# Kernel tuning notes

Measured on AMD Instinct MI355X. Metric: run time of the kernel, lower is better.

The kernel has to match this reference:

```python
import jax, jax.numpy as jnp
import numpy as np

T, B, I, H, O = 512, 64, 256, 512, 256

def setup_inputs() -> dict:
    key = jax.random.key(0)
    ks = jax.random.split(key, 7)
    s_ih = 1.0 / np.sqrt(H)
    return {
        "x": jax.random.normal(ks[0], (T, B, I), dtype=jnp.float32),
        "W_ih": jax.random.uniform(ks[1], (H, I), jnp.float32, -s_ih, s_ih),
        "W_hh": jax.random.uniform(ks[2], (H, H), jnp.float32, -s_ih, s_ih),
        "b_ih": jax.random.uniform(ks[3], (H,), jnp.float32, -s_ih, s_ih),
        "b_hh": jax.random.uniform(ks[4], (H,), jnp.float32, -s_ih, s_ih),
        "W_out": jax.random.uniform(ks[5], (O, H), jnp.float32, -s_ih, s_ih),
        "b_out": jax.random.uniform(ks[6], (O,), jnp.float32, -s_ih, s_ih),
    }

def reference(x, W_ih, W_hh, b_ih, b_hh, W_out, b_out):
    # Precompute input projection for all timesteps: [T, B, H]
    xp = jnp.einsum('tbi,hi->tbh', x, W_ih) + b_ih + b_hh

    def step(h, xp_t):
        h_new = jnp.tanh(xp_t + h @ W_hh.T)
        return h_new, h_new

    h0 = jnp.zeros((x.shape[1], W_hh.shape[0]), dtype=x.dtype)
    h_last, rnn_out = jax.lax.scan(step, h0, xp)  # rnn_out: [T, B, H]
    y = jnp.einsum('tbh,oh->tbo', rnn_out, W_out) + b_out
    return y, h_last[None]  # h: [1, B, H] matching torch nn.RNN
```

## Files before the change

### kernel.cpp

```cpp
#include <hip/hip_runtime.h>

#define T_DIM 512
#define B_DIM 64
#define I_DIM 256
#define H_DIM 512
#define O_DIM 256

typedef __attribute__((ext_vector_type(8))) short short8;
typedef __attribute__((ext_vector_type(4))) float f32x4;

__device__ __forceinline__ unsigned short f2bf(float f){
  unsigned int u = __builtin_bit_cast(unsigned int, f);
  u += 0x7fffu + ((u >> 16) & 1u);
  return (unsigned short)(u >> 16);
}
__device__ __forceinline__ float bf2f(unsigned short b){
  unsigned int u = ((unsigned int)b) << 16;
  return __builtin_bit_cast(float, u);
}

#if defined(__has_builtin)
#if __has_builtin(__builtin_amdgcn_sdot4)
#define HAVE_SDOT4 1
#endif
#if __has_builtin(__builtin_amdgcn_update_dpp)
#define HAVE_DPP 1
#endif
#endif

__device__ __forceinline__ int sdot4(int a, int b, int c){
#ifdef HAVE_SDOT4
  return __builtin_amdgcn_sdot4(a, b, c, false);
#else
  #pragma unroll
  for (int i = 0; i < 4; ++i){
    c += (int)(signed char)(a >> (8*i) & 0xff) * (int)(signed char)(b >> (8*i) & 0xff);
  }
  return c;
#endif
}

__global__ void pack_bf16(const float* __restrict__ x,
                          const float* __restrict__ wih,
                          const float* __restrict__ wout,
                          unsigned short* __restrict__ xb,
                          unsigned short* __restrict__ wihb,
                          unsigned short* __restrict__ woutb){
  const int NX = (T_DIM*B_DIM*I_DIM)/4;
  const int NW = (H_DIM*I_DIM)/4;
  int i = blockIdx.x * 256 + threadIdx.x;
  const float4* src; unsigned short* dst; int j;
  if (i < NX)          { src = (const float4*)x;    dst = xb;    j = i; }
  else if (i < NX+NW)  { src = (const float4*)wih;  dst = wihb;  j = i - NX; }
  else                 { src = (const float4*)wout; dst = woutb; j = i - NX - NW; }
  float4 f = src[j];
  ushort4 v;
  v.x = f2bf(f.x); v.y = f2bf(f.y); v.z = f2bf(f.z); v.w = f2bf(f.w);
  ((ushort4*)dst)[j] = v;
}

__global__ void quant_whh(const float* __restrict__ W, int* __restrict__ Wq){
  int p = blockIdx.x * blockDim.x + threadIdx.x;
  const float s  = 0.04419417382415922f;
  const float qs = 127.0f / s;
  int out = 0;
  #pragma unroll
  for (int i = 0; i < 4; ++i){
    float w = W[(size_t)p*4 + i];
    int q = __float2int_rn(w * qs);
    q = q < -127 ? -127 : (q > 127 ? 127 : q);
    out |= (q & 0xff) << (8*i);
  }
  Wq[p] = out;
}

__global__
__attribute__((amdgpu_flat_work_group_size(512, 512), amdgpu_waves_per_eu(2, 2)))
void rnn_recur(
    const int* __restrict__ Wq,
    const unsigned short* __restrict__ xp,
    unsigned short* __restrict__ rnn,
    float* __restrict__ hlast)
{
  __shared__ union {
    int  hq[2][128];
    char occupancy_cap[84 * 1024];
  } sm;
  const int b   = blockIdx.x;
  const int tid = threadIdx.x;
  const int g   = tid >> 3;
  const int c   = tid & 7;
  const int cc  = c & 3;
  const int rr  = c >> 2;

  int w[4][32];
  #pragma unroll
  for (int i = 0; i < 4; ++i){
    const uint4* wp = (const uint4*)(Wq + (size_t)(8*g + 4*rr + i)*128 + 32*cc);
    #pragma unroll
    for (int k = 0; k < 8; ++k){
      uint4 v = wp[k];
      w[i][4*k+0] = (int)v.x; w[i][4*k+1] = (int)v.y;
      w[i][4*k+2] = (int)v.z; w[i][4*k+3] = (int)v.w;
    }
  }
  if (tid < 256) ((int*)sm.hq)[tid] = 0;

  const int D    = tid >> 2;
  const int wloc = D ^ (((D >> 5) & 3) << 2);

  int ko[8];
  #pragma unroll
  for (int k = 0; k < 8; ++k) ko[k] = 8*cc + (k ^ cc);

  const float kscale = 0.04419417382415922f / (127.0f * 127.0f);
  const int BH = B_DIM * H_DIM;

  float xp_next = bf2f(xp[(size_t)b*H_DIM + tid]);
  float h = 0.0f;
  __syncthreads();

  for (int t = 0; t < T_DIM; ++t){
    float xp_cur = xp_next;
    {
      int tn = (t + 1 < T_DIM) ? (t + 1) : t;
      xp_next = bf2f(xp[(size_t)tn*BH + (size_t)b*H_DIM + tid]);
    }
    const uint4* hb = (const uint4*)sm.hq[t & 1];
    uint4 hv[8];
    #pragma unroll
    for (int k = 0; k < 8; ++k) hv[k] = hb[ko[k]];

    int acc[4];
    #pragma unroll
    for (int i = 0; i < 4; ++i) acc[i] = 0;
    #pragma unroll
    for (int i = 0; i < 4; ++i){
      #pragma unroll
      for (int k = 0; k < 8; ++k){
        acc[i] = sdot4(w[i][4*k+0], (int)hv[k].x, acc[i]);
        acc[i] = sdot4(w[i][4*k+1], (int)hv[k].y, acc[i]);
        acc[i] = sdot4(w[i][4*k+2], (int)hv[k].z, acc[i]);
        acc[i] = sdot4(w[i][4*k+3], (int)hv[k].w, acc[i]);
      }
    }
#ifdef HAVE_DPP
    #pragma unroll
    for (int i = 0; i < 4; ++i){
      acc[i] += __builtin_amdgcn_update_dpp(0, acc[i], 0xB1, 0xf, 0xf, true);
      acc[i] += __builtin_amdgcn_update_dpp(0, acc[i], 0x4E, 0xf, 0xf, true);
    }
#else
    #pragma unroll
    for (int i = 0; i < 4; ++i){
      acc[i] += __shfl_xor(acc[i], 1);
      acc[i] += __shfl_xor(acc[i], 2);
    }
#endif
    int t0 = (c & 1) ? acc[1] : acc[0];
    int t1 = (c & 1) ? acc[3] : acc[2];
    int am = (c & 2) ? t1 : t0;

    float pre = xp_cur + (float)am * kscale;
    float aa = fabsf(pre);
    float e  = __expf(-2.0f * aa);
    float r  = (1.0f - e) * __builtin_amdgcn_rcpf(1.0f + e);
    h = copysignf(r, pre);

    rnn[(size_t)t*BH + (size_t)b*H_DIM + tid] = f2bf(h);

    int q = __float2int_rn(h * 127.0f) & 0xff;
#ifdef HAVE_DPP
    int p1 = __builtin_amdgcn_update_dpp(0, q, 0xB1, 0xf, 0xf, true);
    int y  = q | (p1 << 8);
    int p2 = __builtin_amdgcn_update_dpp(0, y, 0x4E, 0xf, 0xf, true);
    int z  = y | (p2 << 16);
    if ((tid & 3) == 0) sm.hq[(t + 1) & 1][wloc] = z;
#else
    ((char*)sm.hq[(t + 1) & 1])[wloc*4 + (tid & 3)] = (char)q;
#endif
    __syncthreads();
  }
  hlast[(size_t)b*H_DIM + tid] = h;
}

template<typename TA, typename TB, typename TO>
__global__ __launch_bounds__(256) void gemm_bt(
    const TA* __restrict__ A, const TB* __restrict__ B, TO* __restrict__ C,
    const float* __restrict__ bias1, const float* __restrict__ bias2,
    int M, int N, int K)
{
  __shared__ unsigned short As[64][40];
  __shared__ unsigned short Bs[64][40];
  const int tid  = threadIdx.x;
  const int m0   = blockIdx.y * 64;
  const int n0   = blockIdx.x * 64;
  const int srow = tid >> 2, skc = tid & 3;
  const int lane = tid & 63, wid = tid >> 6;
  const int wm   = wid >> 1, wn = wid & 1;
  const int lr   = lane & 15, lq = lane >> 4;

  f32x4 acc[2][2];
  #pragma unroll
  for (int i = 0; i < 2; ++i)
    #pragma unroll
    for (int j = 0; j < 2; ++j) acc[i][j] = (f32x4){0.f, 0.f, 0.f, 0.f};

  for (int k0 = 0; k0 < K; k0 += 32){
    {
      const TA* src = A + (size_t)(m0 + srow)*K + k0 + skc*8;
      uint4 v;
      if constexpr (__is_same(TA, float)){
        float4 f0 = *(const float4*)src;
        float4 f1 = *(const float4*)(src + 4);
        v.x = (unsigned)f2bf(f0.x) | ((unsigned)f2bf(f0.y) << 16);
        v.y = (unsigned)f2bf(f0.z) | ((unsigned)f2bf(f0.w) << 16);
        v.z = (unsigned)f2bf(f1.x) | ((unsigned)f2bf(f1.y) << 16);
        v.w = (unsigned)f2bf(f1.z) | ((unsigned)f2bf(f1.w) << 16);
      } else {
        v = *(const uint4*)src;
      }
      *(uint4*)&As[srow][skc*8] = v;
    }
    {
      const TB* src = B + (size_t)(n0 + srow)*K + k0 + skc*8;
      uint4 v;
      if constexpr (__is_same(TB, float)){
        float4 f0 = *(const float4*)src;
        float4 f1 = *(const float4*)(src + 4);
        v.x = (unsigned)f2bf(f0.x) | ((unsigned)f2bf(f0.y) << 16);
        v.y = (unsigned)f2bf(f0.z) | ((unsigned)f2bf(f0.w) << 16);
        v.z = (unsigned)f2bf(f1.x) | ((unsigned)f2bf(f1.y) << 16);
        v.w = (unsigned)f2bf(f1.z) | ((unsigned)f2bf(f1.w) << 16);
      } else {
        v = *(const uint4*)src;
      }
      *(uint4*)&Bs[srow][skc*8] = v;
    }
    __syncthreads();
    uint4 av0 = *(const uint4*)&As[wm*32      + lr][lq*8];
    uint4 av1 = *(const uint4*)&As[wm*32 + 16 + lr][lq*8];
    uint4 bv0 = *(const uint4*)&Bs[wn*32      + lr][lq*8];
    uint4 bv1 = *(const uint4*)&Bs[wn*32 + 16 + lr][lq*8];
    short8 a0 = __builtin_bit_cast(short8, av0);
    short8 a1 = __builtin_bit_cast(short8, av1);
    short8 b0 = __builtin_bit_cast(short8, bv0);
    short8 b1 = __builtin_bit_cast(short8, bv1);
    acc[0][0] = __builtin_amdgcn_mfma_f32_16x16x32_bf16(a0, b0, acc[0][0], 0, 0, 0);
    acc[0][1] = __builtin_amdgcn_mfma_f32_16x16x32_bf16(a0, b1, acc[0][1], 0, 0, 0);
    acc[1][0] = __builtin_amdgcn_mfma_f32_16x16x32_bf16(a1, b0, acc[1][0], 0, 0, 0);
    acc[1][1] = __builtin_amdgcn_mfma_f32_16x16x32_bf16(a1, b1, acc[1][1], 0, 0, 0);
    __syncthreads();
  }

  #pragma unroll
  for (int i = 0; i < 2; ++i)
    #pragma unroll
    for (int j = 0; j < 2; ++j)
      #pragma unroll
      for (int r = 0; r < 4; ++r){
        int grow = m0 + wm*32 + i*16 + lq*4 + r;
        int gcol = n0 + wn*32 + j*16 + lr;
        float v = acc[i][j][r] + bias1[gcol];
        if (bias2) v += bias2[gcol];
        if constexpr (__is_same(TO, float)) C[(size_t)grow*N + gcol] = v;
        else                                C[(size_t)grow*N + gcol] = f2bf(v);
      }
}

extern "C" void kernel_launch(void* const* d_in, const int* in_sizes, int n_in,
                              void* d_out, int out_size, void* d_ws, size_t ws_size,
                              hipStream_t stream){
  (void)in_sizes; (void)n_in; (void)out_size; (void)ws_size;
  const float* x    = (const float*)d_in[0];
  const float* Wih  = (const float*)d_in[1];
  const float* Whh  = (const float*)d_in[2];
  const float* bih  = (const float*)d_in[3];
  const float* bhh  = (const float*)d_in[4];
  const float* Wout = (const float*)d_in[5];
  const float* bout = (const float*)d_in[6];
  float* y     = (float*)d_out;
  float* hlast = y + (size_t)T_DIM * B_DIM * O_DIM;

  char* ws = (char*)d_ws;
  const size_t MB = 1024*1024;
  unsigned short* xp   = (unsigned short*)ws;
  unsigned short* rnn  = (unsigned short*)(ws + 32*MB);
  unsigned short* xb   = (unsigned short*)(ws + 32*MB);
  unsigned short* wihb = (unsigned short*)(ws + 48*MB);
  int*            Wq   = (int*)           (ws + 64*MB);
  unsigned short* wob  = (unsigned short*)(ws + 64*MB + 256*1024);

  pack_bf16<<<8448, 256, 0, stream>>>(x, Wih, Wout, xb, wihb, wob);
  quant_whh<<<256, 256, 0, stream>>>(Whh, Wq);
  gemm_bt<unsigned short, unsigned short, unsigned short><<<dim3(8, 512), 256, 0, stream>>>(
      xb, wihb, xp, bih, bhh, T_DIM*B_DIM, H_DIM, I_DIM);
  rnn_recur<<<64, 512, 0, stream>>>(Wq, xp, rnn, hlast);
  gemm_bt<unsigned short, unsigned short, float><<<dim3(4, 512), 256, 0, stream>>>(
      rnn, wob, y, bout, nullptr, T_DIM*B_DIM, O_DIM, H_DIM);
}
```

Baseline: 542.6 us.

## Use int8 MFMA for recurrent matvec instead of sdot4 with DPP reduction

Replaces the per-thread sdot4 dot products and DPP cross-lane reductions in the sequential RNN step with int8 16x16x64 MFMA instructions. The quantized W_hh rows are held in registers as MFMA A-fragments, and the hidden state is broadcast as the B operand. Results are picked out of the accumulator lanes and rearranged with a shuffle. Because only one column of each MFMA carries useful data (batch 1 per block), most of the matrix throughput goes unused. The gain depends on cutting per-step latency on the serial critical path.

Result: faster. 524.2 us (-3.4%).

```diff
diff --git a/kernel.cpp b/kernel.cpp
--- a/kernel.cpp
+++ b/kernel.cpp
@@ -8,6 +8,7 @@
 
 typedef __attribute__((ext_vector_type(8))) short short8;
 typedef __attribute__((ext_vector_type(4))) float f32x4;
+typedef __attribute__((ext_vector_type(4))) int   i32x4;
 
 __device__ __forceinline__ unsigned short f2bf(float f){
   unsigned int u = __builtin_bit_cast(unsigned int, f);
@@ -20,25 +21,10 @@
 }
 
 #if defined(__has_builtin)
-#if __has_builtin(__builtin_amdgcn_sdot4)
-#define HAVE_SDOT4 1
-#endif
 #if __has_builtin(__builtin_amdgcn_update_dpp)
 #define HAVE_DPP 1
 #endif
 #endif
-
-__device__ __forceinline__ int sdot4(int a, int b, int c){
-#ifdef HAVE_SDOT4
-  return __builtin_amdgcn_sdot4(a, b, c, false);
-#else
-  #pragma unroll
-  for (int i = 0; i < 4; ++i){
-    c += (int)(signed char)(a >> (8*i) & 0xff) * (int)(signed char)(b >> (8*i) & 0xff);
-  }
-  return c;
-#endif
-}
 
 __global__ void pack_bf16(const float* __restrict__ x,
                           const float* __restrict__ wih,
@@ -83,35 +69,29 @@
     float* __restrict__ hlast)
 {
   __shared__ union {
-    int  hq[2][128];
+    char H[2][512];
     char occupancy_cap[84 * 1024];
   } sm;
-  const int b   = blockIdx.x;
-  const int tid = threadIdx.x;
-  const int g   = tid >> 3;
-  const int c   = tid & 7;
-  const int cc  = c & 3;
-  const int rr  = c >> 2;
-
-  int w[4][32];
-  #pragma unroll
-  for (int i = 0; i < 4; ++i){
-    const uint4* wp = (const uint4*)(Wq + (size_t)(8*g + 4*rr + i)*128 + 32*cc);
-    #pragma unroll
-    for (int k = 0; k < 8; ++k){
-      uint4 v = wp[k];
-      w[i][4*k+0] = (int)v.x; w[i][4*k+1] = (int)v.y;
-      w[i][4*k+2] = (int)v.z; w[i][4*k+3] = (int)v.w;
-    }
-  }
-  if (tid < 256) ((int*)sm.hq)[tid] = 0;
-
-  const int D    = tid >> 2;
-  const int wloc = D ^ (((D >> 5) & 3) << 2);
-
-  int ko[8];
-  #pragma unroll
-  for (int k = 0; k < 8; ++k) ko[k] = 8*cc + (k ^ cc);
+  const int b    = blockIdx.x;
+  const int tid  = threadIdx.x;
+  const int lane = tid & 63;
+  const int wv   = tid >> 6;
+  const int lr   = lane & 15;
+  const int hi   = lane >> 4;
+
+  i32x4 wf[4][8];
+  const char* Wb = (const char*)Wq;
+  #pragma unroll
+  for (int rt = 0; rt < 4; ++rt){
+    const char* rowp = Wb + (size_t)(64*wv + 16*rt + lr)*512 + hi*16;
+    #pragma unroll
+    for (int kt = 0; kt < 8; ++kt)
+      wf[rt][kt] = *(const i32x4*)(rowp + (size_t)kt*64);
+  }
+
+  if (tid < 256) ((int*)sm.H)[tid] = 0;
+
+  const int src = (((lane >> 2) & 3) << 4) | ((lane >> 4) << 2) | (lane & 3);
 
   const float kscale = 0.04419417382415922f / (127.0f * 127.0f);
   const int BH = B_DIM * H_DIM;
@@ -126,40 +106,37 @@
       int tn = (t + 1 < T_DIM) ? (t + 1) : t;
       xp_next = bf2f(xp[(size_t)tn*BH + (size_t)b*H_DIM + tid]);
     }
-    const uint4* hb = (const uint4*)sm.hq[t & 1];
-    uint4 hv[8];
-    #pragma unroll
-    for (int k = 0; k < 8; ++k) hv[k] = hb[ko[k]];
-
-    int acc[4];
-    #pragma unroll
-    for (int i = 0; i < 4; ++i) acc[i] = 0;
-    #pragma unroll
-    for (int i = 0; i < 4; ++i){
-      #pragma unroll
-      for (int k = 0; k < 8; ++k){
-        acc[i] = sdot4(w[i][4*k+0], (int)hv[k].x, acc[i]);
-        acc[i] = sdot4(w[i][4*k+1], (int)hv[k].y, acc[i]);
-        acc[i] = sdot4(w[i][4*k+2], (int)hv[k].z, acc[i]);
-        acc[i] = sdot4(w[i][4*k+3], (int)hv[k].w, acc[i]);
-      }
-    }
-#ifdef HAVE_DPP
-    #pragma unroll
-    for (int i = 0; i < 4; ++i){
-      acc[i] += __builtin_amdgcn_update_dpp(0, acc[i], 0xB1, 0xf, 0xf, true);
-      acc[i] += __builtin_amdgcn_update_dpp(0, acc[i], 0x4E, 0xf, 0xf, true);
-    }
-#else
-    #pragma unroll
-    for (int i = 0; i < 4; ++i){
-      acc[i] += __shfl_xor(acc[i], 1);
-      acc[i] += __shfl_xor(acc[i], 2);
-    }
-#endif
-    int t0 = (c & 1) ? acc[1] : acc[0];
-    int t1 = (c & 1) ? acc[3] : acc[2];
-    int am = (c & 2) ? t1 : t0;
+
+    const char* Hc = sm.H[t & 1];
+    i32x4 a0 = {0,0,0,0}, a1 = {0,0,0,0}, a2 = {0,0,0,0}, a3 = {0,0,0,0};
+    #pragma unroll
+    for (int kt = 0; kt < 8; ++kt){
+      i32x4 bf = *(const i32x4*)(Hc + kt*64 + hi*16);
+      a0 = __builtin_amdgcn_mfma_i32_16x16x64_i8(wf[0][kt], bf, a0, 0, 0, 0);
+      a1 = __builtin_amdgcn_mfma_i32_16x16x64_i8(wf[1][kt], bf, a1, 0, 0, 0);
+      a2 = __builtin_amdgcn_mfma_i32_16x16x64_i8(wf[2][kt], bf, a2, 0, 0, 0);
+      a3 = __builtin_amdgcn_mfma_i32_16x16x64_i8(wf[3][kt], bf, a3, 0, 0, 0);
+    }
+
+    int f0, f1, f2, f3;
+    {
+      int e0 = (lane & 4) ? a1[0] : a0[0];
+      int e1 = (lane & 4) ? a3[0] : a2[0];
+      f0 = (lane & 8) ? e1 : e0;
+      e0 = (lane & 4) ? a1[1] : a0[1];
+      e1 = (lane & 4) ? a3[1] : a2[1];
+      f1 = (lane & 8) ? e1 : e0;
+      e0 = (lane & 4) ? a1[2] : a0[2];
+      e1 = (lane & 4) ? a3[2] : a2[2];
+      f2 = (lane & 8) ? e1 : e0;
+      e0 = (lane & 4) ? a1[3] : a0[3];
+      e1 = (lane & 4) ? a3[3] : a2[3];
+      f3 = (lane & 8) ? e1 : e0;
+    }
+    int g0 = (lane & 1) ? f1 : f0;
+    int g1 = (lane & 1) ? f3 : f2;
+    int am0 = (lane & 2) ? g1 : g0;
+    int am  = __shfl(am0, src);
 
     float pre = xp_cur + (float)am * kscale;
     float aa = fabsf(pre);
@@ -175,9 +152,9 @@
     int y  = q | (p1 << 8);
     int p2 = __builtin_amdgcn_update_dpp(0, y, 0x4E, 0xf, 0xf, true);
     int z  = y | (p2 << 16);
-    if ((tid & 3) == 0) sm.hq[(t + 1) & 1][wloc] = z;
+    if ((tid & 3) == 0) ((int*)sm.H[(t + 1) & 1])[tid >> 2] = z;
 #else
-    ((char*)sm.hq[(t + 1) & 1])[wloc*4 + (tid & 3)] = (char)q;
+    sm.H[(t + 1) & 1][tid] = (char)q;
 #endif
     __syncthreads();
   }
```
